# Kernel tuning notes

Measured on AMD Instinct MI355X. Metric: run time of the kernel, lower is better.

## Reference

```python
import jax, jax.numpy as jnp
import numpy as np

DIM = 192
HEADS = 6
WIN = (2, 6, 12)          # (pl, lat, lon)
TOW = 64                  # type_of_windows = (8//2)*(96//6)
N_TOK = WIN[0] * WIN[1] * WIN[2]            # 144
TABLE_ROWS = WIN[0]**2 * WIN[1]**2 * (2 * WIN[2] - 1)  # 3312


def calc_position_bias_indices(size):
    pl, la, lo = size
    plq = np.arange(pl); plk = -np.arange(pl) * pl
    laq = np.arange(la); lak = -np.arange(la) * la
    lon = np.arange(lo)
    gq = np.stack(np.meshgrid(plq, laq, lon, indexing='ij'))  # [3,pl,la,lo]
    gk = np.stack(np.meshgrid(plk, lak, lon, indexing='ij'))
    fq = gq.reshape(3, -1)
    fk = gk.reshape(3, -1)
    d = fq[:, :, None] - fk[:, None, :]          # [3,N,N]
    d = np.transpose(d, (1, 2, 0)).copy()
    d[:, :, 2] += lo - 1
    d[:, :, 1] *= 2 * lo - 1
    d[:, :, 0] *= (2 * lo - 1) * la * la
    return d.sum(-1)                              # [N,N]


def setup_inputs() -> dict:
    key = jax.random.key(0)
    ks = jax.random.split(key, 7)
    B_, nW, N, C = 15, TOW, N_TOK, DIM
    x = jax.random.normal(ks[0], (B_, nW, N, C), jnp.float32)
    mask = jax.random.normal(ks[1], (15, nW, N, N), jnp.float32)  # nLon=15
    qkv_w = jax.random.normal(ks[2], (3 * C, C), jnp.float32) * 0.02
    qkv_b = jnp.zeros((3 * C,), jnp.float32)
    table = jax.random.normal(ks[3], (TABLE_ROWS, TOW, HEADS), jnp.float32) * 0.02
    proj_w = jax.random.normal(ks[4], (C, C), jnp.float32) * 0.02
    proj_b = jnp.zeros((C,), jnp.float32)
    pos_index = jnp.asarray(calc_position_bias_indices(WIN), jnp.int32)  # [N,N]
    return {"x": x, "mask": mask, "qkv_w": qkv_w, "qkv_b": qkv_b,
            "table": table, "proj_w": proj_w, "proj_b": proj_b,
            "pos_index": pos_index}


def reference(x, mask, qkv_w, qkv_b, table, proj_w, proj_b, pos_index):
    B_, nW, N, C = x.shape
    h = HEADS
    hd = C // h
    scale = hd ** -0.5
    # qkv projection -> (3, B_, h, nW, N, hd)
    qkv = (jnp.einsum('bwnc,dc->bwnd', x, qkv_w) + qkv_b)
    qkv = qkv.reshape(B_, nW, N, 3, h, hd).transpose(3, 0, 4, 1, 2, 5)
    q, k, v = qkv[0] * scale, qkv[1], qkv[2]
    attn = jnp.einsum('bhwqd,bhwkd->bhwqk', q, k)      # [B_,h,nW,N,N]
    # gather earth position bias: [N,N,tow,h] -> [h,tow,N,N]
    bias = table[pos_index.reshape(-1)].reshape(N, N, nW, h)
    bias = bias.transpose(3, 2, 0, 1)
    attn = attn + bias[None]
    nLon = mask.shape[0]
    attn = attn.reshape(B_ // nLon, nLon, h, nW, N, N) + mask[None, :, None]
    attn = attn.reshape(B_, h, nW, N, N)
    attn = jax.nn.softmax(attn, axis=-1)
    out = jnp.einsum('bhwqk,bhwkd->bhwqd', attn, v)
    out = out.transpose(0, 2, 3, 1, 4).reshape(B_, nW, N, C)
    return jnp.einsum('bwnc,dc->bwnd', out, proj_w) + proj_b
```

## Files before the change

### kernel.cpp

```cpp
#include <hip/hip_runtime.h>

#define HEADS 6
#define N_TOK 144
#define DIM   192
#define NW    64
#define NB    15
#define NBW   (NB * NW)

typedef __attribute__((ext_vector_type(8))) short bf16x8;
typedef __attribute__((ext_vector_type(4))) float f32x4;

#define MFMA(a, b, c) __builtin_amdgcn_mfma_f32_16x16x32_bf16(a, b, c, 0, 0, 0)

static __device__ __forceinline__ short f2bf(float f) {
    union { float f; unsigned u; } v; v.f = f;
    unsigned r = v.u + 0x7FFFu + ((v.u >> 16) & 1u);
    return (short)(r >> 16);
}
static __device__ __forceinline__ float bf2f(short s) {
    union { unsigned u; float f; } v;
    v.u = ((unsigned)(unsigned short)s) << 16;
    return v.f;
}
static __device__ __forceinline__ unsigned pk2(float a, float b) {
    return (unsigned)(unsigned short)f2bf(a) |
           ((unsigned)(unsigned short)f2bf(b) << 16);
}

__global__ __launch_bounds__(256)
void bias_k(const float* __restrict__ table, const int* __restrict__ pos_index,
            short* __restrict__ bias_bf) {
    const int t = blockIdx.x;
    for (int e = threadIdx.x; e < N_TOK * N_TOK; e += 256) {
        int idx = pos_index[e];
        bias_bf[(long)t * (N_TOK * N_TOK) + e] = f2bf(table[(long)idx * 384 + t]);
    }
}

__global__ __launch_bounds__(256)
void cvt_k(const float* __restrict__ w, short* __restrict__ o, int n) {
    int i = blockIdx.x * 256 + threadIdx.x;
    if (i < n) o[i] = f2bf(w[i]);
}

__global__ __launch_bounds__(576, 4)
void fused_k(const float* __restrict__ x, const short* __restrict__ qkvw_bf,
             const float* __restrict__ qkv_b, const short* __restrict__ bias_bf,
             const float* __restrict__ mask, short* __restrict__ tmp) {
    __shared__ short klds[N_TOK * 40];
    __shared__ short vlds[32 * 152];
    __shared__ short pws[9 * 16 * 40];

    const int bw  = blockIdx.x;
    const int tid = threadIdx.x;
    const int lane = tid & 63, lq = lane & 15, lg = lane >> 4;
    const int wid = tid >> 6;
    const int m0 = wid * 16;
    const int q  = m0 + lq;
    const int w  = bw & 63;
    const float scale = 0.17677669529663687f;

    bf16x8 af[6];
    {
        const float* xg = x + ((long)bw * N_TOK + q) * DIM;
        #pragma unroll
        for (int ks = 0; ks < 6; ++ks) {
            const float4* p = (const float4*)&xg[ks * 32 + 8 * lg];
            float4 f0 = p[0], f1 = p[1];
            bf16x8 a;
            a[0]=f2bf(f0.x); a[1]=f2bf(f0.y); a[2]=f2bf(f0.z); a[3]=f2bf(f0.w);
            a[4]=f2bf(f1.x); a[5]=f2bf(f1.y); a[6]=f2bf(f1.z); a[7]=f2bf(f1.w);
            af[ks] = a;
        }
    }

    short* pw = pws + wid * 16 * 40;
    short* tb = tmp + ((long)bw * N_TOK + q) * DIM;
    const float* mp = mask + (long)bw * (N_TOK * N_TOK) + q * N_TOK + 4 * lg;
    const f32x4 zf = {};
    const bf16x8 zb = {};

    #pragma unroll 1
    for (int h = 0; h < HEADS; ++h) {
        f32x4 acc[3][2] = {};
        #pragma unroll
        for (int sel = 0; sel < 3; ++sel) {
            const short* wb = qkvw_bf + ((long)sel * 192 + h * 32) * 192;
            #pragma unroll
            for (int ks = 0; ks < 6; ++ks) {
                #pragma unroll
                for (int nt = 0; nt < 2; ++nt) {
                    bf16x8 b = *(const bf16x8*)&wb[(nt * 16 + lq) * 192 + ks * 32 + 8 * lg];
                    acc[sel][nt] = MFMA(af[ks], b, acc[sel][nt]);
                }
            }
        }

        #pragma unroll
        for (int nt = 0; nt < 2; ++nt) {
            float bb = qkv_b[h * 32 + nt * 16 + lq];
            #pragma unroll
            for (int i = 0; i < 4; ++i)
                pw[(4 * lg + i) * 40 + nt * 16 + lq] =
                    f2bf((acc[0][nt][i] + bb) * scale);
        }

        __syncthreads();

        #pragma unroll
        for (int nt = 0; nt < 2; ++nt) {
            float bk = qkv_b[192 + h * 32 + nt * 16 + lq];
            float bv = qkv_b[384 + h * 32 + nt * 16 + lq];
            #pragma unroll
            for (int i = 0; i < 4; ++i) {
                klds[(m0 + 4 * lg + i) * 40 + nt * 16 + lq] = f2bf(acc[1][nt][i] + bk);
                vlds[(nt * 16 + lq) * 152 + m0 + 4 * lg + i] = f2bf(acc[2][nt][i] + bv);
            }
        }
        __syncthreads();

        bf16x8 bq = *(const bf16x8*)&pw[lq * 40 + 8 * lg];
        f32x4 lgt[9];
        #pragma unroll
        for (int nt = 0; nt < 9; ++nt) {
            bf16x8 ak = *(const bf16x8*)&klds[(nt * 16 + lq) * 40 + 8 * lg];
            lgt[nt] = MFMA(ak, bq, zf);
        }

        const short* bp = bias_bf + (long)(w * 6 + h) * (N_TOK * N_TOK)
                        + q * N_TOK + 4 * lg;
        #pragma unroll
        for (int nt = 0; nt < 9; ++nt) {
            short4 bs = *(const short4*)&bp[nt * 16];
            float4 mf = *(const float4*)&mp[nt * 16];
            lgt[nt][0] += bf2f(bs.x) + mf.x;
            lgt[nt][1] += bf2f(bs.y) + mf.y;
            lgt[nt][2] += bf2f(bs.z) + mf.z;
            lgt[nt][3] += bf2f(bs.w) + mf.w;
        }

        float m = lgt[0][0];
        #pragma unroll
        for (int nt = 0; nt < 9; ++nt)
            #pragma unroll
            for (int i = 0; i < 4; ++i) m = fmaxf(m, lgt[nt][i]);
        m = fmaxf(m, __shfl_xor(m, 16));
        m = fmaxf(m, __shfl_xor(m, 32));
        float s = 0.f;
        #pragma unroll
        for (int nt = 0; nt < 9; ++nt)
            #pragma unroll
            for (int i = 0; i < 4; ++i) {
                float p = __expf(lgt[nt][i] - m);
                lgt[nt][i] = p;
                s += p;
            }
        s += __shfl_xor(s, 16);
        s += __shfl_xor(s, 32);
        const float inv = 1.f / s;

        f32x4 o[2] = {};
        #pragma unroll
        for (int kt = 0; kt < 5; ++kt) {
            const int nt0 = 2 * kt;
            *(unsigned*)&pw[lq * 40 + 4 * lg]     = pk2(lgt[nt0][0], lgt[nt0][1]);
            *(unsigned*)&pw[lq * 40 + 4 * lg + 2] = pk2(lgt[nt0][2], lgt[nt0][3]);
            if (kt < 4) {
                const int nt1 = nt0 + 1;
                *(unsigned*)&pw[lq * 40 + 16 + 4 * lg]     = pk2(lgt[nt1][0], lgt[nt1][1]);
                *(unsigned*)&pw[lq * 40 + 16 + 4 * lg + 2] = pk2(lgt[nt1][2], lgt[nt1][3]);
            }
            bf16x8 bpf = *(const bf16x8*)&pw[lq * 40 + 8 * lg];
            #pragma unroll
            for (int et = 0; et < 2; ++et) {
                bf16x8 av = *(const bf16x8*)&vlds[(et * 16 + lq) * 152 + kt * 32 + 8 * lg];
                bf16x8 aa = av, bb = bpf;
                if (kt == 4 && lg >= 2) { aa = zb; bb = zb; }
                o[et] = MFMA(aa, bb, o[et]);
            }
        }

        #pragma unroll
        for (int et = 0; et < 2; ++et) {
            short4 sx = { f2bf(o[et][0] * inv), f2bf(o[et][1] * inv),
                          f2bf(o[et][2] * inv), f2bf(o[et][3] * inv) };
            *(short4*)&tb[h * 32 + et * 16 + 4 * lg] = sx;
        }
    }
}

__global__ __launch_bounds__(192)
void proj_k(const short* __restrict__ tmp, const short* __restrict__ pwt,
            const float* __restrict__ proj_b, float* __restrict__ out) {
    const int bid = blockIdx.x;
    const int mthird = bid % 3;
    const int bw = bid / 3;
    const int tid = threadIdx.x;
    const int wid = tid >> 6, lane = tid & 63, lq = lane & 15, lg = lane >> 4;
    const int m0 = (mthird * 3 + wid) * 16;
    const short* tb = tmp + (long)bw * N_TOK * DIM;

    f32x4 acc[12] = {};
    for (int ks = 0; ks < 6; ++ks) {
        const int k0 = ks * 32 + 8 * lg;
        bf16x8 a = *(const bf16x8*)&tb[(m0 + lq) * DIM + k0];
        #pragma unroll
        for (int nt = 0; nt < 12; ++nt) {
            bf16x8 b = *(const bf16x8*)&pwt[(nt * 16 + lq) * DIM + k0];
            acc[nt] = MFMA(a, b, acc[nt]);
        }
    }
    float* ob = out + (long)bw * N_TOK * DIM;
    #pragma unroll
    for (int nt = 0; nt < 12; ++nt) {
        float pb = proj_b[nt * 16 + lq];
        #pragma unroll
        for (int i = 0; i < 4; ++i)
            ob[(m0 + 4 * lg + i) * DIM + nt * 16 + lq] = acc[nt][i] + pb;
    }
}

extern "C" void kernel_launch(void* const* d_in, const int* in_sizes, int n_in,
                              void* d_out, int out_size, void* d_ws, size_t ws_size,
                              hipStream_t stream) {
    const float* x        = (const float*)d_in[0];
    const float* mask     = (const float*)d_in[1];
    const float* qkv_w    = (const float*)d_in[2];
    const float* qkv_b    = (const float*)d_in[3];
    const float* table    = (const float*)d_in[4];
    const float* proj_w   = (const float*)d_in[5];
    const float* proj_b   = (const float*)d_in[6];
    const int*   pos_index= (const int*)d_in[7];
    float* out = (float*)d_out;

    short* bias_bf  = (short*)d_ws;
    short* projw_bf = bias_bf + (size_t)384 * N_TOK * N_TOK;
    short* qkvw_bf  = projw_bf + 36864;
    short* tmp_ws   = qkvw_bf + 110592;

    bias_k<<<384, 256, 0, stream>>>(table, pos_index, bias_bf);
    cvt_k<<<144, 256, 0, stream>>>(proj_w, projw_bf, DIM * DIM);
    cvt_k<<<432, 256, 0, stream>>>(qkv_w, qkvw_bf, 3 * DIM * DIM);

    fused_k<<<NBW, 576, 0, stream>>>(x, qkvw_bf, qkv_b, bias_bf, mask, tmp_ws);
    proj_k<<<NBW * 3, 192, 0, stream>>>(tmp_ws, projw_bf, proj_b, out);
}
```

Baseline: 523.5 us.

## Fuse output projection into attention kernel and remap block order

Folds the output projection into the attention kernel, so the per-head attention outputs stay in a shared-memory buffer instead of round-tripping through a global bf16 workspace and a second launch. It also preloads the mask into registers before the head loop, pads the V LDS stride, reorders the QKV weight loop, and permutes block indices so that blocks sharing a window index are spread apart. The cost is a much larger LDS footprint (about 57KB of outb plus the existing buffers), a lower launch-bounds occupancy hint (2 instead of 4), and more register pressure from the mask registers and the 12 projection accumulators.

```diff
diff --git a/kernel.cpp b/kernel.cpp
--- a/kernel.cpp
+++ b/kernel.cpp
@@ -43,15 +43,18 @@
     if (i < n) o[i] = f2bf(w[i]);
 }
 
-__global__ __launch_bounds__(576, 4)
-void fused_k(const float* __restrict__ x, const short* __restrict__ qkvw_bf,
-             const float* __restrict__ qkv_b, const short* __restrict__ bias_bf,
-             const float* __restrict__ mask, short* __restrict__ tmp) {
+__global__ __launch_bounds__(576, 2)
+void fused64_k(const float* __restrict__ x, const short* __restrict__ qkvw_bf,
+               const float* __restrict__ qkv_b, const short* __restrict__ bias_bf,
+               const float* __restrict__ mask, const short* __restrict__ pwt,
+               const float* __restrict__ proj_b, float* __restrict__ out) {
     __shared__ short klds[N_TOK * 40];
-    __shared__ short vlds[32 * 152];
+    __shared__ short vlds[32 * 156];
     __shared__ short pws[9 * 16 * 40];
-
-    const int bw  = blockIdx.x;
+    __shared__ short outb[N_TOK * 200];
+
+    const int p  = blockIdx.x;
+    const int bw = (p & 7) * 120 + (p >> 3);
     const int tid = threadIdx.x;
     const int lane = tid & 63, lq = lane & 15, lg = lane >> 4;
     const int wid = tid >> 6;
@@ -65,8 +68,8 @@
         const float* xg = x + ((long)bw * N_TOK + q) * DIM;
         #pragma unroll
         for (int ks = 0; ks < 6; ++ks) {
-            const float4* p = (const float4*)&xg[ks * 32 + 8 * lg];
-            float4 f0 = p[0], f1 = p[1];
+            const float4* pp = (const float4*)&xg[ks * 32 + 8 * lg];
+            float4 f0 = pp[0], f1 = pp[1];
             bf16x8 a;
             a[0]=f2bf(f0.x); a[1]=f2bf(f0.y); a[2]=f2bf(f0.z); a[3]=f2bf(f0.w);
             a[4]=f2bf(f1.x); a[5]=f2bf(f1.y); a[6]=f2bf(f1.z); a[7]=f2bf(f1.w);
@@ -74,9 +77,14 @@
         }
     }
 
+    float4 mreg[9];
+    {
+        const float* mp = mask + (long)bw * (N_TOK * N_TOK) + q * N_TOK + 4 * lg;
+        #pragma unroll
+        for (int nt = 0; nt < 9; ++nt) mreg[nt] = *(const float4*)&mp[nt * 16];
+    }
+
     short* pw = pws + wid * 16 * 40;
-    short* tb = tmp + ((long)bw * N_TOK + q) * DIM;
-    const float* mp = mask + (long)bw * (N_TOK * N_TOK) + q * N_TOK + 4 * lg;
     const f32x4 zf = {};
     const bf16x8 zb = {};
 
@@ -84,17 +92,15 @@
     for (int h = 0; h < HEADS; ++h) {
         f32x4 acc[3][2] = {};
         #pragma unroll
-        for (int sel = 0; sel < 3; ++sel) {
-            const short* wb = qkvw_bf + ((long)sel * 192 + h * 32) * 192;
-            #pragma unroll
-            for (int ks = 0; ks < 6; ++ks) {
+        for (int ks = 0; ks < 6; ++ks)
+            #pragma unroll
+            for (int sel = 0; sel < 3; ++sel)
                 #pragma unroll
                 for (int nt = 0; nt < 2; ++nt) {
-                    bf16x8 b = *(const bf16x8*)&wb[(nt * 16 + lq) * 192 + ks * 32 + 8 * lg];
+                    bf16x8 b = *(const bf16x8*)&qkvw_bf[
+                        ((long)sel * 192 + h * 32 + nt * 16 + lq) * 192 + ks * 32 + 8 * lg];
                     acc[sel][nt] = MFMA(af[ks], b, acc[sel][nt]);
                 }
-            }
-        }
 
         #pragma unroll
         for (int nt = 0; nt < 2; ++nt) {
@@ -106,7 +112,6 @@
         }
 
         __syncthreads();
-
         #pragma unroll
         for (int nt = 0; nt < 2; ++nt) {
             float bk = qkv_b[192 + h * 32 + nt * 16 + lq];
@@ -114,7 +119,7 @@
             #pragma unroll
             for (int i = 0; i < 4; ++i) {
                 klds[(m0 + 4 * lg + i) * 40 + nt * 16 + lq] = f2bf(acc[1][nt][i] + bk);
-                vlds[(nt * 16 + lq) * 152 + m0 + 4 * lg + i] = f2bf(acc[2][nt][i] + bv);
+                vlds[(nt * 16 + lq) * 156 + m0 + 4 * lg + i] = f2bf(acc[2][nt][i] + bv);
             }
         }
         __syncthreads();
@@ -132,11 +137,10 @@
         #pragma unroll
         for (int nt = 0; nt < 9; ++nt) {
             short4 bs = *(const short4*)&bp[nt * 16];
-            float4 mf = *(const float4*)&mp[nt * 16];
-            lgt[nt][0] += bf2f(bs.x) + mf.x;
-            lgt[nt][1] += bf2f(bs.y) + mf.y;
-            lgt[nt][2] += bf2f(bs.z) + mf.z;
-            lgt[nt][3] += bf2f(bs.w) + mf.w;
+            lgt[nt][0] += bf2f(bs.x) + mreg[nt].x;
+            lgt[nt][1] += bf2f(bs.y) + mreg[nt].y;
+            lgt[nt][2] += bf2f(bs.z) + mreg[nt].z;
+            lgt[nt][3] += bf2f(bs.w) + mreg[nt].w;
         }
 
         float m = lgt[0][0];
@@ -151,9 +155,9 @@
         for (int nt = 0; nt < 9; ++nt)
             #pragma unroll
             for (int i = 0; i < 4; ++i) {
-                float p = __expf(lgt[nt][i] - m);
-                lgt[nt][i] = p;
-                s += p;
+                float pe = __expf(lgt[nt][i] - m);
+                lgt[nt][i] = pe;
+                s += pe;
             }
         s += __shfl_xor(s, 16);
         s += __shfl_xor(s, 32);
@@ -173,7 +177,7 @@
             bf16x8 bpf = *(const bf16x8*)&pw[lq * 40 + 8 * lg];
             #pragma unroll
             for (int et = 0; et < 2; ++et) {
-                bf16x8 av = *(const bf16x8*)&vlds[(et * 16 + lq) * 152 + kt * 32 + 8 * lg];
+                bf16x8 av = *(const bf16x8*)&vlds[(et * 16 + lq) * 156 + kt * 32 + 8 * lg];
                 bf16x8 aa = av, bb = bpf;
                 if (kt == 4 && lg >= 2) { aa = zb; bb = zb; }
                 o[et] = MFMA(aa, bb, o[et]);
@@ -184,26 +188,16 @@
         for (int et = 0; et < 2; ++et) {
             short4 sx = { f2bf(o[et][0] * inv), f2bf(o[et][1] * inv),
                           f2bf(o[et][2] * inv), f2bf(o[et][3] * inv) };
-            *(short4*)&tb[h * 32 + et * 16 + 4 * lg] = sx;
-        }
-    }
-}
-
-__global__ __launch_bounds__(192)
-void proj_k(const short* __restrict__ tmp, const short* __restrict__ pwt,
-            const float* __restrict__ proj_b, float* __restrict__ out) {
-    const int bid = blockIdx.x;
-    const int mthird = bid % 3;
-    const int bw = bid / 3;
-    const int tid = threadIdx.x;
-    const int wid = tid >> 6, lane = tid & 63, lq = lane & 15, lg = lane >> 4;
-    const int m0 = (mthird * 3 + wid) * 16;
-    const short* tb = tmp + (long)bw * N_TOK * DIM;
+            *(short4*)&outb[q * 200 + h * 32 + et * 16 + 4 * lg] = sx;
+        }
+    }
+    __syncthreads();
 
     f32x4 acc[12] = {};
+    #pragma unroll
     for (int ks = 0; ks < 6; ++ks) {
         const int k0 = ks * 32 + 8 * lg;
-        bf16x8 a = *(const bf16x8*)&tb[(m0 + lq) * DIM + k0];
+        bf16x8 a = *(const bf16x8*)&outb[(m0 + lq) * 200 + k0];
         #pragma unroll
         for (int nt = 0; nt < 12; ++nt) {
             bf16x8 b = *(const bf16x8*)&pwt[(nt * 16 + lq) * DIM + k0];
@@ -236,12 +230,11 @@
     short* bias_bf  = (short*)d_ws;
     short* projw_bf = bias_bf + (size_t)384 * N_TOK * N_TOK;
     short* qkvw_bf  = projw_bf + 36864;
-    short* tmp_ws   = qkvw_bf + 110592;
 
     bias_k<<<384, 256, 0, stream>>>(table, pos_index, bias_bf);
     cvt_k<<<144, 256, 0, stream>>>(proj_w, projw_bf, DIM * DIM);
     cvt_k<<<432, 256, 0, stream>>>(qkv_w, qkvw_bf, 3 * DIM * DIM);
 
-    fused_k<<<NBW, 576, 0, stream>>>(x, qkvw_bf, qkv_b, bias_bf, mask, tmp_ws);
-    proj_k<<<NBW * 3, 192, 0, stream>>>(tmp_ws, projw_bf, proj_b, out);
-}
+    fused64_k<<<NBW, 576, 0, stream>>>(x, qkvw_bf, qkv_b, bias_bf, mask,
+                                       projw_bf, proj_b, out);
+}
```

New measurement: 505.3 us. 3.5% less time.
